# Kernel optimization log

Hardware: AMD Instinct MI355X
Metric: run time of the kernel (lower is better)

Reference implementation:

```python
import jax, jax.numpy as jnp
import numpy as np

N = 50000      # nodes
E = 800000     # edges
C = 128        # dim_feat / channels
D = 256        # dim_dense
OUT = 2        # dim_out
L = 5          # num_layers - 1 GCN2Conv layers
ALPHA = 0.1    # main_param -> GCN2Conv alpha; theta=None -> beta=1.0
SLOPE = 0.01   # LeakyReLU default negative slope


def setup_inputs() -> dict:
    key = jax.random.key(0)
    ks = jax.random.split(key, 6)
    x = jax.random.normal(ks[0], (N, C), jnp.float32)
    edge_index = jax.random.randint(ks[1], (2, E), 0, N, jnp.int32)
    conv_weights = jax.random.normal(ks[2], (L, C, C), jnp.float32) * (1.0 / np.sqrt(C))
    w_dense = jax.random.normal(ks[3], (C, D), jnp.float32) * (1.0 / np.sqrt(C))
    b_dense = jnp.zeros((D,), jnp.float32)
    w_out = jax.random.normal(ks[4], (D, OUT), jnp.float32) * (1.0 / np.sqrt(D))
    b_out = jnp.zeros((OUT,), jnp.float32)
    return dict(x=x, edge_index=edge_index, conv_weights=conv_weights,
                w_dense=w_dense, b_dense=b_dense, w_out=w_out, b_out=b_out)


def _gcn_norm(edge_index, num_nodes):
    """Symmetric gcn_norm with self-loops: returns row, col, D^-1/2 * D^-1/2 edge weights."""
    loop = jnp.arange(num_nodes, dtype=edge_index.dtype)
    row = jnp.concatenate([edge_index[0], loop])  # sources
    col = jnp.concatenate([edge_index[1], loop])  # targets (aggregation index)
    ones = jnp.ones(row.shape[0], jnp.float32)
    deg = jax.ops.segment_sum(ones, col, num_segments=num_nodes)
    dinv = jnp.where(deg > 0, jax.lax.rsqrt(jnp.maximum(deg, 1e-12)), 0.0)
    return row, col, dinv[row] * dinv[col]


def reference(x, edge_index, conv_weights, w_dense, b_dense, w_out, b_out):
    num_nodes = x.shape[0]
    row, col, norm = _gcn_norm(edge_index, num_nodes)
    x0 = x
    for l in range(conv_weights.shape[0]):
        # propagate: h[i] = sum_{j->i} norm * x[j]   (gather -> scatter-add)
        h = jax.ops.segment_sum(norm[:, None] * x[row], col, num_segments=num_nodes)
        # GCN2Conv with shared_weights=True, beta=1 (theta=None): out = ((1-a)h + a*x0) @ W
        out = (1.0 - ALPHA) * h + ALPHA * x0
        x = jax.nn.leaky_relu(out @ conv_weights[l], negative_slope=SLOPE)
    x = x @ w_dense + b_dense
    return x @ w_out + b_out
```

## Files before the change

kernel.cpp:

```cpp
#include <hip/hip_runtime.h>
#include <hip/hip_fp16.h>

#define C 128
#define NOUT 2
#define ALPHA 0.1f
#define SLOPE 0.01f
#define ZP 136

typedef _Float16 half4v __attribute__((ext_vector_type(4)));
typedef float float4v __attribute__((ext_vector_type(4)));


__global__ void count_kernel(const int* __restrict__ col, int* __restrict__ cnt,
                             int* __restrict__ rank, int E) {
    int e = blockIdx.x * 256 + threadIdx.x;
    if (e < E) rank[e] = atomicAdd(&cnt[col[e]], 1);
}

__global__ __launch_bounds__(1024) void scanA_kernel(const int* __restrict__ cnt,
                                                     int* __restrict__ offs,
                                                     int* __restrict__ bsum,
                                                     float* __restrict__ dinv, int n) {
    __shared__ int wsum[16];
    int t = threadIdx.x, lane = t & 63, wv = t >> 6;
    int i = blockIdx.x * 1024 + t;
    int v = (i < n) ? cnt[i] : 0;
    if (i < n) dinv[i] = rsqrtf((float)(v + 1));
    int sc = v;
    #pragma unroll
    for (int d = 1; d < 64; d <<= 1) {
        int u = __shfl_up(sc, d);
        if (lane >= d) sc += u;
    }
    if (lane == 63) wsum[wv] = sc;
    __syncthreads();
    int woff = 0;
    #pragma unroll
    for (int j = 0; j < 16; ++j) woff += (j < wv) ? wsum[j] : 0;
    if (i < n) offs[i] = woff + sc - v;
    if (t == 0) {
        int tot = 0;
        #pragma unroll
        for (int j = 0; j < 16; ++j) tot += wsum[j];
        bsum[blockIdx.x] = tot;
    }
}

__global__ __launch_bounds__(1024) void scanB_kernel(const int* __restrict__ bsum,
                                                     int* __restrict__ bbase, int nb) {
    __shared__ int wsum[16];
    int t = threadIdx.x, lane = t & 63, wv = t >> 6;
    int v = (t < nb) ? bsum[t] : 0;
    int sc = v;
    #pragma unroll
    for (int d = 1; d < 64; d <<= 1) {
        int u = __shfl_up(sc, d);
        if (lane >= d) sc += u;
    }
    if (lane == 63) wsum[wv] = sc;
    __syncthreads();
    int woff = 0;
    #pragma unroll
    for (int j = 0; j < 16; ++j) woff += (j < wv) ? wsum[j] : 0;
    if (t < nb) bbase[t] = woff + sc - v;
}

__global__ void scanC_kernel(int* __restrict__ offs, const int* __restrict__ bbase,
                             int n, int E) {
    int i = blockIdx.x * 256 + threadIdx.x;
    if (i < n) offs[i] = offs[i] + bbase[i >> 10];
    if (i == n) offs[n] = E;
}

__global__ void fill_kernel(const int* __restrict__ row, const int* __restrict__ col,
                            const float* __restrict__ dinv, const int* __restrict__ offs,
                            const int* __restrict__ rank, unsigned* __restrict__ csr, int E) {
    int base = blockIdx.x * 2048 + threadIdx.x;
    #pragma unroll
    for (int j = 0; j < 8; ++j) {
        int e = base + j * 256;
        if (e < E) {
            int r = row[e], c = col[e];
            union { __half h; unsigned short u; } nh;
            nh.h = __float2half_rn(dinv[r] * dinv[c]);
            csr[offs[c] + rank[e]] = ((unsigned)r << 16) | (unsigned)nh.u;
        }
    }
}

__global__ __launch_bounds__(256) void convert_kernel(const float* __restrict__ x,
                                                      __half* __restrict__ xh, int n) {
    int g = blockIdx.x * 256 + threadIdx.x;
    if (g >= n * 32) return;
    float4 v = ((const float4*)x)[g];
    union { __half2 h; unsigned u; } a, b;
    a.h = __float22half2_rn(make_float2(v.x, v.y));
    b.h = __float22half2_rn(make_float2(v.z, v.w));
    ((uint2*)xh)[g] = make_uint2(a.u, b.u);
}

__global__ void wtc_kernel(const float* __restrict__ W, _Float16* __restrict__ WT, int total) {
    int idx = blockIdx.x * 256 + threadIdx.x;
    if (idx >= total) return;
    int l = idx >> 14, rem = idx & 16383;
    int nrow = rem >> 7, kk = rem & 127;
    WT[idx] = (_Float16)W[(l << 14) + kk * C + nrow];
}

__global__ void wdc_kernel(const float* __restrict__ wd, _Float16* __restrict__ WDT) {
    int idx = blockIdx.x * 256 + threadIdx.x;
    if (idx >= 256 * C) return;
    int nrow = idx >> 7, kk = idx & 127;
    WDT[idx] = (_Float16)wd[kk * 256 + nrow];
}

__device__ __forceinline__ void accum8(float* a, uint4 q, float w) {
    union { unsigned u; __half2 h; } c;
    float2 f;
    c.u = q.x; f = __half22float2(c.h); a[0] += w * f.x; a[1] += w * f.y;
    c.u = q.y; f = __half22float2(c.h); a[2] += w * f.x; a[3] += w * f.y;
    c.u = q.z; f = __half22float2(c.h); a[4] += w * f.x; a[5] += w * f.y;
    c.u = q.w; f = __half22float2(c.h); a[6] += w * f.x; a[7] += w * f.y;
}

__device__ __forceinline__ uint4 pack8(const float* a) {
    union { __half2 h; unsigned u; } c0, c1, c2, c3;
    c0.h = __float22half2_rn(make_float2(a[0], a[1]));
    c1.h = __float22half2_rn(make_float2(a[2], a[3]));
    c2.h = __float22half2_rn(make_float2(a[4], a[5]));
    c3.h = __float22half2_rn(make_float2(a[6], a[7]));
    return make_uint4(c0.u, c1.u, c2.u, c3.u);
}

__device__ __forceinline__ float norm_of(unsigned m) {
    union { unsigned short u; __half h; } nh;
    nh.u = (unsigned short)(m & 0xffffu);
    return __half2float(nh.h);
}

__global__ __launch_bounds__(256) void agg_kernel(
    const __half* __restrict__ xc, const __half* __restrict__ x0h,
    const int* __restrict__ offs, const unsigned* __restrict__ csr,
    const float* __restrict__ dinv, __half* __restrict__ z, int n)
{
    int node = blockIdx.x * 8 + (threadIdx.x >> 5);
    if (node >= n) return;
    int l32 = threadIdx.x & 31;
    int sub = l32 >> 4;
    int cg = l32 & 15;
    const uint4* x4 = (const uint4*)xc;
    float a0[8] = {}, a1[8] = {}, a2[8] = {}, a3[8] = {};
    int beg = offs[node], end = offs[node + 1];
    int k = beg + sub;
    for (; k + 14 < end; k += 16) {
        unsigned m0 = csr[k], m1 = csr[k + 2], m2 = csr[k + 4], m3 = csr[k + 6];
        unsigned m4 = csr[k + 8], m5 = csr[k + 10], m6 = csr[k + 12], m7 = csr[k + 14];
        uint4 q0 = x4[(size_t)(m0 >> 16) * 16 + cg];
        uint4 q1 = x4[(size_t)(m1 >> 16) * 16 + cg];
        uint4 q2 = x4[(size_t)(m2 >> 16) * 16 + cg];
        uint4 q3 = x4[(size_t)(m3 >> 16) * 16 + cg];
        uint4 q4 = x4[(size_t)(m4 >> 16) * 16 + cg];
        uint4 q5 = x4[(size_t)(m5 >> 16) * 16 + cg];
        uint4 q6 = x4[(size_t)(m6 >> 16) * 16 + cg];
        uint4 q7 = x4[(size_t)(m7 >> 16) * 16 + cg];
        accum8(a0, q0, norm_of(m0));
        accum8(a1, q1, norm_of(m1));
        accum8(a2, q2, norm_of(m2));
        accum8(a3, q3, norm_of(m3));
        accum8(a0, q4, norm_of(m4));
        accum8(a1, q5, norm_of(m5));
        accum8(a2, q6, norm_of(m6));
        accum8(a3, q7, norm_of(m7));
    }
    for (; k + 6 < end; k += 8) {
        unsigned m0 = csr[k], m1 = csr[k + 2], m2 = csr[k + 4], m3 = csr[k + 6];
        uint4 q0 = x4[(size_t)(m0 >> 16) * 16 + cg];
        uint4 q1 = x4[(size_t)(m1 >> 16) * 16 + cg];
        uint4 q2 = x4[(size_t)(m2 >> 16) * 16 + cg];
        uint4 q3 = x4[(size_t)(m3 >> 16) * 16 + cg];
        accum8(a0, q0, norm_of(m0));
        accum8(a1, q1, norm_of(m1));
        accum8(a2, q2, norm_of(m2));
        accum8(a3, q3, norm_of(m3));
    }
    for (; k < end; k += 2) {
        unsigned m = csr[k];
        uint4 q = x4[(size_t)(m >> 16) * 16 + cg];
        accum8(a0, q, norm_of(m));
    }
    #pragma unroll
    for (int j = 0; j < 8; ++j) a0[j] += a1[j] + a2[j] + a3[j];
    #pragma unroll
    for (int j = 0; j < 8; ++j) a0[j] += __shfl_xor(a0[j], 16);
    if (sub == 0) {
        float di = dinv[node], sw = di * di;
        uint4 qs = x4[(size_t)node * 16 + cg];
        accum8(a0, qs, sw);
        uint4 q0x = ((const uint4*)x0h)[(size_t)node * 16 + cg];
        float xr[8] = {};
        accum8(xr, q0x, 1.f);
        float zz[8];
        #pragma unroll
        for (int j = 0; j < 8; ++j) zz[j] = (1.f - ALPHA) * a0[j] + ALPHA * xr[j];
        ((uint4*)z)[(size_t)node * 16 + cg] = pack8(zz);
    }
}

__global__ __launch_bounds__(256) void layer_mfma(
    const __half* __restrict__ zin, const _Float16* __restrict__ WT,
    __half* __restrict__ xn, int n)
{
    __shared__ _Float16 zl[64 * ZP];
    __shared__ _Float16 ol[64 * ZP];
    int i0 = blockIdx.x * 64;
    int t = threadIdx.x;
    int w = t >> 6, lane = t & 63;
    int c = lane & 15, g = lane >> 4;

    const uint4* z4 = (const uint4*)zin;
    for (int p = t; p < 64 * 16; p += 256) {
        int r = p >> 4, c8 = p & 15;
        uint4 zv = make_uint4(0, 0, 0, 0);
        if (i0 + r < n) zv = z4[(size_t)(i0 + r) * 16 + c8];
        *(uint4*)&zl[r * ZP + c8 * 8] = zv;
    }

    half4v bf[8][2];
    #pragma unroll
    for (int kb = 0; kb < 8; ++kb)
        #pragma unroll
        for (int nt = 0; nt < 2; ++nt)
            bf[kb][nt] = *(const half4v*)&WT[((w * 2 + nt) * 16 + c) * C + kb * 16 + 4 * g];

    __syncthreads();

    #pragma unroll
    for (int m = 0; m < 4; ++m) {
        const _Float16* arow = &zl[(m * 16 + c) * ZP];
        half4v af[8];
        #pragma unroll
        for (int kb = 0; kb < 8; ++kb) af[kb] = *(const half4v*)&arow[kb * 16 + 4 * g];
        float4v acc0 = (float4v)0.f, acc1 = (float4v)0.f;
        #pragma unroll
        for (int kb = 0; kb < 8; ++kb) {
            acc0 = __builtin_amdgcn_mfma_f32_16x16x16f16(af[kb], bf[kb][0], acc0, 0, 0, 0);
            acc1 = __builtin_amdgcn_mfma_f32_16x16x16f16(af[kb], bf[kb][1], acc1, 0, 0, 0);
        }
        #pragma unroll
        for (int r = 0; r < 4; ++r) {
            float v0 = acc0[r]; v0 = v0 > 0.f ? v0 : SLOPE * v0;
            float v1 = acc1[r]; v1 = v1 > 0.f ? v1 : SLOPE * v1;
            ol[(m * 16 + 4 * g + r) * ZP + (w * 2 + 0) * 16 + c] = (_Float16)v0;
            ol[(m * 16 + 4 * g + r) * ZP + (w * 2 + 1) * 16 + c] = (_Float16)v1;
        }
    }
    __syncthreads();
    for (int p = t; p < 64 * 16; p += 256) {
        int r = p >> 4, c8 = p & 15;
        int node = i0 + r;
        if (node < n)
            ((uint4*)xn)[(size_t)node * 16 + c8] = *(uint4*)&ol[r * ZP + c8 * 8];
    }
}

__global__ __launch_bounds__(256) void dense_mfma(
    const __half* __restrict__ xin, const _Float16* __restrict__ WDT,
    const float* __restrict__ bd, const float* __restrict__ wo,
    const float* __restrict__ bo, float* __restrict__ out, int n)
{
    __shared__ _Float16 xl[64 * ZP];
    __shared__ float pp[64][4][2];
    int i0 = blockIdx.x * 64;
    int t = threadIdx.x;
    int w = t >> 6, lane = t & 63;
    int c = lane & 15, g = lane >> 4;

    const uint4* g4 = (const uint4*)xin;
    for (int p = t; p < 64 * 16; p += 256) {
        int r = p >> 4, c8 = p & 15;
        uint4 v = make_uint4(0, 0, 0, 0);
        if (i0 + r < n) v = g4[(size_t)(i0 + r) * 16 + c8];
        *(uint4*)&xl[r * ZP + c8 * 8] = v;
    }

    half4v bf[8][4];
    #pragma unroll
    for (int kb = 0; kb < 8; ++kb)
        #pragma unroll
        for (int nt = 0; nt < 4; ++nt)
            bf[kb][nt] = *(const half4v*)&WDT[((w * 4 + nt) * 16 + c) * C + kb * 16 + 4 * g];
    float bdv[4], wo0[4], wo1[4];
    #pragma unroll
    for (int nt = 0; nt < 4; ++nt) {
        int coln = (w * 4 + nt) * 16 + c;
        bdv[nt] = bd[coln];
        wo0[nt] = wo[coln * 2 + 0];
        wo1[nt] = wo[coln * 2 + 1];
    }

    __syncthreads();

    #pragma unroll
    for (int m = 0; m < 4; ++m) {
        const _Float16* arow = &xl[(m * 16 + c) * ZP];
        half4v af[8];
        #pragma unroll
        for (int kb = 0; kb < 8; ++kb) af[kb] = *(const half4v*)&arow[kb * 16 + 4 * g];
        float4v acc[4];
        #pragma unroll
        for (int nt = 0; nt < 4; ++nt) acc[nt] = (float4v)0.f;
        #pragma unroll
        for (int kb = 0; kb < 8; ++kb) {
            #pragma unroll
            for (int nt = 0; nt < 4; ++nt)
                acc[nt] = __builtin_amdgcn_mfma_f32_16x16x16f16(af[kb], bf[kb][nt], acc[nt], 0, 0, 0);
        }
        float p0[4] = {0.f, 0.f, 0.f, 0.f}, p1[4] = {0.f, 0.f, 0.f, 0.f};
        #pragma unroll
        for (int nt = 0; nt < 4; ++nt) {
            #pragma unroll
            for (int r = 0; r < 4; ++r) {
                float hv = acc[nt][r] + bdv[nt];
                p0[r] += hv * wo0[nt];
                p1[r] += hv * wo1[nt];
            }
        }
        #pragma unroll
        for (int ms = 1; ms <= 8; ms <<= 1) {
            #pragma unroll
            for (int r = 0; r < 4; ++r) {
                p0[r] += __shfl_xor(p0[r], ms);
                p1[r] += __shfl_xor(p1[r], ms);
            }
        }
        if (c == 0) {
            #pragma unroll
            for (int r = 0; r < 4; ++r) {
                pp[m * 16 + 4 * g + r][w][0] = p0[r];
                pp[m * 16 + 4 * g + r][w][1] = p1[r];
            }
        }
    }
    __syncthreads();
    if (t < 128) {
        int r = t >> 1, o = t & 1;
        int node = i0 + r;
        if (node < n) {
            float s = pp[r][0][o] + pp[r][1][o] + pp[r][2][o] + pp[r][3][o];
            out[(size_t)node * NOUT + o] = s + bo[o];
        }
    }
}

extern "C" void kernel_launch(void* const* d_in, const int* in_sizes, int n_in,
                              void* d_out, int out_size, void* d_ws, size_t ws_size,
                              hipStream_t stream) {
    const float* x0    = (const float*)d_in[0];
    const int*   ei    = (const int*)d_in[1];
    const float* convW = (const float*)d_in[2];
    const float* wd    = (const float*)d_in[3];
    const float* bd    = (const float*)d_in[4];
    const float* wo    = (const float*)d_in[5];
    const float* bo    = (const float*)d_in[6];
    float* out = (float*)d_out;

    int N = in_sizes[0] / C;
    int E = in_sizes[1] / 2;
    int L = in_sizes[2] / (C * C);
    const int* row = ei;
    const int* col = ei + E;
    int NB = (N + 1023) / 1024;

    char* p = (char*)d_ws;
    auto alloc = [&](size_t bytes) {
        char* r = p;
        p += (bytes + 255) & ~(size_t)255;
        return r;
    };
    int*      cnt    = (int*)alloc((size_t)N * 4);
    int*      offs   = (int*)alloc((size_t)(N + 1) * 4);
    int*      rank   = (int*)alloc((size_t)E * 4);
    int*      bsum   = (int*)alloc((size_t)NB * 4);
    int*      bbase  = (int*)alloc((size_t)NB * 4);
    unsigned* csr    = (unsigned*)alloc((size_t)E * 4);
    float*    dinv   = (float*)alloc((size_t)N * 4);
    __half*   x0h    = (__half*)alloc((size_t)N * C * 2);
    __half*   bufA   = (__half*)alloc((size_t)N * C * 2);
    __half*   zbuf   = (__half*)alloc((size_t)N * C * 2);
    _Float16* WT     = (_Float16*)alloc((size_t)L * C * C * 2);
    _Float16* WDT    = (_Float16*)alloc((size_t)256 * C * 2);

    hipMemsetAsync(cnt, 0, (size_t)N * 4, stream);
    count_kernel<<<(E + 255) / 256, 256, 0, stream>>>(col, cnt, rank, E);
    scanA_kernel<<<NB, 1024, 0, stream>>>(cnt, offs, bsum, dinv, N);
    scanB_kernel<<<1, 1024, 0, stream>>>(bsum, bbase, NB);
    scanC_kernel<<<(N + 256) / 256, 256, 0, stream>>>(offs, bbase, N, E);
    fill_kernel<<<(E + 2047) / 2048, 256, 0, stream>>>(row, col, dinv, offs, rank, csr, E);
    convert_kernel<<<(N * 32 + 255) / 256, 256, 0, stream>>>(x0, x0h, N);
    int wtot = L * C * C;
    wtc_kernel<<<(wtot + 255) / 256, 256, 0, stream>>>(convW, WT, wtot);
    wdc_kernel<<<(256 * C + 255) / 256, 256, 0, stream>>>(wd, WDT);

    const __half* xc = x0h;
    for (int l = 0; l < L; ++l) {
        agg_kernel<<<(N + 7) / 8, 256, 0, stream>>>(xc, x0h, offs, csr, dinv, zbuf, N);
        layer_mfma<<<(N + 63) / 64, 256, 0, stream>>>(zbuf, WT + (size_t)l * C * C,
                                                      bufA, N);
        xc = bufA;
    }
    dense_mfma<<<(N + 63) / 64, 256, 0, stream>>>(xc, WDT, bd, wo, bo, out, N);
}
```

Measured before the change: 365.8 us.

## Merge prep kernels, hoist agg self loads, widen layer_mfma to 512 threads

Folds the scan-finalize, fp32-to-fp16 conversion and both weight-transpose kernels into one prep launch that picks its role by block index, removing three launches. In the aggregation kernel the self-row, x0 row and dinv loads are issued before the edge loop so their latency overlaps the gathers. layer_mfma moves to 512 threads with 8 waves, each computing one 16-column tile instead of two, which trades per-wave MFMA work and register use for more waves per block.

```diff
diff --git a/kernel.cpp b/kernel.cpp
--- a/kernel.cpp
+++ b/kernel.cpp
@@ -65,11 +65,38 @@
     if (t < nb) bbase[t] = woff + sc - v;
 }
 
-__global__ void scanC_kernel(int* __restrict__ offs, const int* __restrict__ bbase,
-                             int n, int E) {
-    int i = blockIdx.x * 256 + threadIdx.x;
-    if (i < n) offs[i] = offs[i] + bbase[i >> 10];
-    if (i == n) offs[n] = E;
+__global__ __launch_bounds__(256) void prep_kernel(
+    int* __restrict__ offs, const int* __restrict__ bbase, int n, int E,
+    const float* __restrict__ x, __half* __restrict__ xh,
+    const float* __restrict__ W, _Float16* __restrict__ WT, int wtot,
+    const float* __restrict__ wd, _Float16* __restrict__ WDT,
+    int SC, int CV, int WTB)
+{
+    int b = blockIdx.x;
+    if (b < SC) {
+        int i = b * 256 + threadIdx.x;
+        if (i < n) offs[i] = offs[i] + bbase[i >> 10];
+        if (i == n) offs[n] = E;
+    } else if (b < SC + CV) {
+        int g = (b - SC) * 256 + threadIdx.x;
+        if (g >= n * 32) return;
+        float4 v = ((const float4*)x)[g];
+        union { __half2 h; unsigned u; } a2, b2;
+        a2.h = __float22half2_rn(make_float2(v.x, v.y));
+        b2.h = __float22half2_rn(make_float2(v.z, v.w));
+        ((uint2*)xh)[g] = make_uint2(a2.u, b2.u);
+    } else if (b < SC + CV + WTB) {
+        int idx = (b - SC - CV) * 256 + threadIdx.x;
+        if (idx >= wtot) return;
+        int l = idx >> 14, rem = idx & 16383;
+        int nrow = rem >> 7, kk = rem & 127;
+        WT[idx] = (_Float16)W[(l << 14) + kk * C + nrow];
+    } else {
+        int idx = (b - SC - CV - WTB) * 256 + threadIdx.x;
+        if (idx >= 256 * C) return;
+        int nrow = idx >> 7, kk = idx & 127;
+        WDT[idx] = (_Float16)wd[kk * 256 + nrow];
+    }
 }
 
 __global__ void fill_kernel(const int* __restrict__ row, const int* __restrict__ col,
@@ -86,32 +113,6 @@
             csr[offs[c] + rank[e]] = ((unsigned)r << 16) | (unsigned)nh.u;
         }
     }
-}
-
-__global__ __launch_bounds__(256) void convert_kernel(const float* __restrict__ x,
-                                                      __half* __restrict__ xh, int n) {
-    int g = blockIdx.x * 256 + threadIdx.x;
-    if (g >= n * 32) return;
-    float4 v = ((const float4*)x)[g];
-    union { __half2 h; unsigned u; } a, b;
-    a.h = __float22half2_rn(make_float2(v.x, v.y));
-    b.h = __float22half2_rn(make_float2(v.z, v.w));
-    ((uint2*)xh)[g] = make_uint2(a.u, b.u);
-}
-
-__global__ void wtc_kernel(const float* __restrict__ W, _Float16* __restrict__ WT, int total) {
-    int idx = blockIdx.x * 256 + threadIdx.x;
-    if (idx >= total) return;
-    int l = idx >> 14, rem = idx & 16383;
-    int nrow = rem >> 7, kk = rem & 127;
-    WT[idx] = (_Float16)W[(l << 14) + kk * C + nrow];
-}
-
-__global__ void wdc_kernel(const float* __restrict__ wd, _Float16* __restrict__ WDT) {
-    int idx = blockIdx.x * 256 + threadIdx.x;
-    if (idx >= 256 * C) return;
-    int nrow = idx >> 7, kk = idx & 127;
-    WDT[idx] = (_Float16)wd[kk * 256 + nrow];
 }
 
 __device__ __forceinline__ void accum8(float* a, uint4 q, float w) {
@@ -149,6 +150,10 @@
     int sub = l32 >> 4;
     int cg = l32 & 15;
     const uint4* x4 = (const uint4*)xc;
+    uint4 qs = x4[(size_t)node * 16 + cg];
+    uint4 q0x = ((const uint4*)x0h)[(size_t)node * 16 + cg];
+    float di = dinv[node];
+
     float a0[8] = {}, a1[8] = {}, a2[8] = {}, a3[8] = {};
     int beg = offs[node], end = offs[node + 1];
     int k = beg + sub;
@@ -193,10 +198,8 @@
     #pragma unroll
     for (int j = 0; j < 8; ++j) a0[j] += __shfl_xor(a0[j], 16);
     if (sub == 0) {
-        float di = dinv[node], sw = di * di;
-        uint4 qs = x4[(size_t)node * 16 + cg];
+        float sw = di * di;
         accum8(a0, qs, sw);
-        uint4 q0x = ((const uint4*)x0h)[(size_t)node * 16 + cg];
         float xr[8] = {};
         accum8(xr, q0x, 1.f);
         float zz[8];
@@ -206,7 +209,7 @@
     }
 }
 
-__global__ __launch_bounds__(256) void layer_mfma(
+__global__ __launch_bounds__(512) void layer_mfma(
     const __half* __restrict__ zin, const _Float16* __restrict__ WT,
     __half* __restrict__ xn, int n)
 {
@@ -218,19 +221,18 @@
     int c = lane & 15, g = lane >> 4;
 
     const uint4* z4 = (const uint4*)zin;
-    for (int p = t; p < 64 * 16; p += 256) {
+    #pragma unroll
+    for (int p = t; p < 64 * 16; p += 512) {
         int r = p >> 4, c8 = p & 15;
         uint4 zv = make_uint4(0, 0, 0, 0);
         if (i0 + r < n) zv = z4[(size_t)(i0 + r) * 16 + c8];
         *(uint4*)&zl[r * ZP + c8 * 8] = zv;
     }
 
-    half4v bf[8][2];
+    half4v bf[8];
     #pragma unroll
     for (int kb = 0; kb < 8; ++kb)
-        #pragma unroll
-        for (int nt = 0; nt < 2; ++nt)
-            bf[kb][nt] = *(const half4v*)&WT[((w * 2 + nt) * 16 + c) * C + kb * 16 + 4 * g];
+        bf[kb] = *(const half4v*)&WT[(w * 16 + c) * C + kb * 16 + 4 * g];
 
     __syncthreads();
 
@@ -240,22 +242,20 @@
         half4v af[8];
         #pragma unroll
         for (int kb = 0; kb < 8; ++kb) af[kb] = *(const half4v*)&arow[kb * 16 + 4 * g];
-        float4v acc0 = (float4v)0.f, acc1 = (float4v)0.f;
-        #pragma unroll
-        for (int kb = 0; kb < 8; ++kb) {
-            acc0 = __builtin_amdgcn_mfma_f32_16x16x16f16(af[kb], bf[kb][0], acc0, 0, 0, 0);
-            acc1 = __builtin_amdgcn_mfma_f32_16x16x16f16(af[kb], bf[kb][1], acc1, 0, 0, 0);
-        }
+        float4v acc = (float4v)0.f;
+        #pragma unroll
+        for (int kb = 0; kb < 8; ++kb)
+            acc = __builtin_amdgcn_mfma_f32_16x16x16f16(af[kb], bf[kb], acc, 0, 0, 0);
         #pragma unroll
         for (int r = 0; r < 4; ++r) {
-            float v0 = acc0[r]; v0 = v0 > 0.f ? v0 : SLOPE * v0;
-            float v1 = acc1[r]; v1 = v1 > 0.f ? v1 : SLOPE * v1;
-            ol[(m * 16 + 4 * g + r) * ZP + (w * 2 + 0) * 16 + c] = (_Float16)v0;
-            ol[(m * 16 + 4 * g + r) * ZP + (w * 2 + 1) * 16 + c] = (_Float16)v1;
-        }
-    }
-    __syncthreads();
-    for (int p = t; p < 64 * 16; p += 256) {
+            float v = acc[r];
+            v = v > 0.f ? v : SLOPE * v;
+            ol[(m * 16 + 4 * g + r) * ZP + w * 16 + c] = (_Float16)v;
+        }
+    }
+    __syncthreads();
+    #pragma unroll
+    for (int p = t; p < 64 * 16; p += 512) {
         int r = p >> 4, c8 = p & 15;
         int node = i0 + r;
         if (node < n)
@@ -394,17 +394,19 @@
     count_kernel<<<(E + 255) / 256, 256, 0, stream>>>(col, cnt, rank, E);
     scanA_kernel<<<NB, 1024, 0, stream>>>(cnt, offs, bsum, dinv, N);
     scanB_kernel<<<1, 1024, 0, stream>>>(bsum, bbase, NB);
-    scanC_kernel<<<(N + 256) / 256, 256, 0, stream>>>(offs, bbase, N, E);
+    int wtot = L * C * C;
+    int SC  = (N + 256) / 256;
+    int CV  = (N * 32 + 255) / 256;
+    int WTB = (wtot + 255) / 256;
+    int WDB = (256 * C + 255) / 256;
+    prep_kernel<<<SC + CV + WTB + WDB, 256, 0, stream>>>(
+        offs, bbase, N, E, x0, x0h, convW, WT, wtot, wd, WDT, SC, CV, WTB);
     fill_kernel<<<(E + 2047) / 2048, 256, 0, stream>>>(row, col, dinv, offs, rank, csr, E);
-    convert_kernel<<<(N * 32 + 255) / 256, 256, 0, stream>>>(x0, x0h, N);
-    int wtot = L * C * C;
-    wtc_kernel<<<(wtot + 255) / 256, 256, 0, stream>>>(convW, WT, wtot);
-    wdc_kernel<<<(256 * C + 255) / 256, 256, 0, stream>>>(wd, WDT);
 
     const __half* xc = x0h;
     for (int l = 0; l < L; ++l) {
         agg_kernel<<<(N + 7) / 8, 256, 0, stream>>>(xc, x0h, offs, csr, dinv, zbuf, N);
-        layer_mfma<<<(N + 63) / 64, 256, 0, stream>>>(zbuf, WT + (size_t)l * C * C,
+        layer_mfma<<<(N + 63) / 64, 512, 0, stream>>>(zbuf, WT + (size_t)l * C * C,
                                                       bufA, N);
         xc = bufA;
     }
```

Result: no change. 366.0 us (+0.1%).

## Merge setup kernels into one launch, hoist self loads, store layer output directly

Applied to the files above, without the earlier changes.

Folds the edge counting, x-to-half conversion and the two weight transposes into a single multi-role kernel, dispatched by block index, to cut three launches from the prologue. The aggregation kernel now issues its self-row, x0-row and dinv loads before the edge loop so their latency overlaps the gathers. The layer GEMM kernel drops its output shared-memory staging and second barrier and writes half values straight to global memory. Those direct writes are scattered 2-byte stores rather than coalesced 16-byte rows, which can raise write traffic inefficiency.

```diff
diff --git a/kernel.cpp b/kernel.cpp
--- a/kernel.cpp
+++ b/kernel.cpp
@@ -11,10 +11,41 @@
 typedef float float4v __attribute__((ext_vector_type(4)));
 
 
-__global__ void count_kernel(const int* __restrict__ col, int* __restrict__ cnt,
-                             int* __restrict__ rank, int E) {
-    int e = blockIdx.x * 256 + threadIdx.x;
-    if (e < E) rank[e] = atomicAdd(&cnt[col[e]], 1);
+__global__ __launch_bounds__(256) void count_prep_kernel(
+    const int* __restrict__ col, int* __restrict__ cnt, int* __restrict__ rank, int E,
+    const float* __restrict__ x, __half* __restrict__ xh, int n,
+    const float* __restrict__ W, _Float16* __restrict__ WT, int wtot,
+    const float* __restrict__ wd, _Float16* __restrict__ WDT,
+    int CB, int CV, int WTB)
+{
+    int b = blockIdx.x;
+    if (b < CB) {
+        int base = b * 1024 + threadIdx.x;
+        #pragma unroll
+        for (int j = 0; j < 4; ++j) {
+            int e = base + j * 256;
+            if (e < E) rank[e] = atomicAdd(&cnt[col[e]], 1);
+        }
+    } else if (b < CB + CV) {
+        int g = (b - CB) * 256 + threadIdx.x;
+        if (g >= n * 32) return;
+        float4 v = ((const float4*)x)[g];
+        union { __half2 h; unsigned u; } a2, b2;
+        a2.h = __float22half2_rn(make_float2(v.x, v.y));
+        b2.h = __float22half2_rn(make_float2(v.z, v.w));
+        ((uint2*)xh)[g] = make_uint2(a2.u, b2.u);
+    } else if (b < CB + CV + WTB) {
+        int idx = (b - CB - CV) * 256 + threadIdx.x;
+        if (idx >= wtot) return;
+        int l = idx >> 14, rem = idx & 16383;
+        int nrow = rem >> 7, kk = rem & 127;
+        WT[idx] = (_Float16)W[(l << 14) + kk * C + nrow];
+    } else {
+        int idx = (b - CB - CV - WTB) * 256 + threadIdx.x;
+        if (idx >= 256 * C) return;
+        int nrow = idx >> 7, kk = idx & 127;
+        WDT[idx] = (_Float16)wd[kk * 256 + nrow];
+    }
 }
 
 __global__ __launch_bounds__(1024) void scanA_kernel(const int* __restrict__ cnt,
@@ -86,32 +117,6 @@
             csr[offs[c] + rank[e]] = ((unsigned)r << 16) | (unsigned)nh.u;
         }
     }
-}
-
-__global__ __launch_bounds__(256) void convert_kernel(const float* __restrict__ x,
-                                                      __half* __restrict__ xh, int n) {
-    int g = blockIdx.x * 256 + threadIdx.x;
-    if (g >= n * 32) return;
-    float4 v = ((const float4*)x)[g];
-    union { __half2 h; unsigned u; } a, b;
-    a.h = __float22half2_rn(make_float2(v.x, v.y));
-    b.h = __float22half2_rn(make_float2(v.z, v.w));
-    ((uint2*)xh)[g] = make_uint2(a.u, b.u);
-}
-
-__global__ void wtc_kernel(const float* __restrict__ W, _Float16* __restrict__ WT, int total) {
-    int idx = blockIdx.x * 256 + threadIdx.x;
-    if (idx >= total) return;
-    int l = idx >> 14, rem = idx & 16383;
-    int nrow = rem >> 7, kk = rem & 127;
-    WT[idx] = (_Float16)W[(l << 14) + kk * C + nrow];
-}
-
-__global__ void wdc_kernel(const float* __restrict__ wd, _Float16* __restrict__ WDT) {
-    int idx = blockIdx.x * 256 + threadIdx.x;
-    if (idx >= 256 * C) return;
-    int nrow = idx >> 7, kk = idx & 127;
-    WDT[idx] = (_Float16)wd[kk * 256 + nrow];
 }
 
 __device__ __forceinline__ void accum8(float* a, uint4 q, float w) {
@@ -149,6 +154,10 @@
     int sub = l32 >> 4;
     int cg = l32 & 15;
     const uint4* x4 = (const uint4*)xc;
+    uint4 qs = x4[(size_t)node * 16 + cg];
+    uint4 q0x = ((const uint4*)x0h)[(size_t)node * 16 + cg];
+    float di = dinv[node];
+
     float a0[8] = {}, a1[8] = {}, a2[8] = {}, a3[8] = {};
     int beg = offs[node], end = offs[node + 1];
     int k = beg + sub;
@@ -193,10 +202,8 @@
     #pragma unroll
     for (int j = 0; j < 8; ++j) a0[j] += __shfl_xor(a0[j], 16);
     if (sub == 0) {
-        float di = dinv[node], sw = di * di;
-        uint4 qs = x4[(size_t)node * 16 + cg];
+        float sw = di * di;
         accum8(a0, qs, sw);
-        uint4 q0x = ((const uint4*)x0h)[(size_t)node * 16 + cg];
         float xr[8] = {};
         accum8(xr, q0x, 1.f);
         float zz[8];
@@ -211,13 +218,13 @@
     __half* __restrict__ xn, int n)
 {
     __shared__ _Float16 zl[64 * ZP];
-    __shared__ _Float16 ol[64 * ZP];
     int i0 = blockIdx.x * 64;
     int t = threadIdx.x;
     int w = t >> 6, lane = t & 63;
     int c = lane & 15, g = lane >> 4;
 
     const uint4* z4 = (const uint4*)zin;
+    #pragma unroll
     for (int p = t; p < 64 * 16; p += 256) {
         int r = p >> 4, c8 = p & 15;
         uint4 zv = make_uint4(0, 0, 0, 0);
@@ -248,18 +255,14 @@
         }
         #pragma unroll
         for (int r = 0; r < 4; ++r) {
-            float v0 = acc0[r]; v0 = v0 > 0.f ? v0 : SLOPE * v0;
-            float v1 = acc1[r]; v1 = v1 > 0.f ? v1 : SLOPE * v1;
-            ol[(m * 16 + 4 * g + r) * ZP + (w * 2 + 0) * 16 + c] = (_Float16)v0;
-            ol[(m * 16 + 4 * g + r) * ZP + (w * 2 + 1) * 16 + c] = (_Float16)v1;
-        }
-    }
-    __syncthreads();
-    for (int p = t; p < 64 * 16; p += 256) {
-        int r = p >> 4, c8 = p & 15;
-        int node = i0 + r;
-        if (node < n)
-            ((uint4*)xn)[(size_t)node * 16 + c8] = *(uint4*)&ol[r * ZP + c8 * 8];
+            int node = i0 + m * 16 + 4 * g + r;
+            if (node < n) {
+                float v0 = acc0[r]; v0 = v0 > 0.f ? v0 : SLOPE * v0;
+                float v1 = acc1[r]; v1 = v1 > 0.f ? v1 : SLOPE * v1;
+                xn[(size_t)node * C + w * 32 + c]      = __float2half_rn(v0);
+                xn[(size_t)node * C + w * 32 + 16 + c] = __float2half_rn(v1);
+            }
+        }
     }
 }
 
@@ -390,16 +393,19 @@
     _Float16* WT     = (_Float16*)alloc((size_t)L * C * C * 2);
     _Float16* WDT    = (_Float16*)alloc((size_t)256 * C * 2);
 
+    int wtot = L * C * C;
+    int CB  = (E + 1023) / 1024;
+    int CV  = (N * 32 + 255) / 256;
+    int WTB = (wtot + 255) / 256;
+    int WDB = (256 * C + 255) / 256;
+
     hipMemsetAsync(cnt, 0, (size_t)N * 4, stream);
-    count_kernel<<<(E + 255) / 256, 256, 0, stream>>>(col, cnt, rank, E);
+    count_prep_kernel<<<CB + CV + WTB + WDB, 256, 0, stream>>>(
+        col, cnt, rank, E, x0, x0h, N, convW, WT, wtot, wd, WDT, CB, CV, WTB);
     scanA_kernel<<<NB, 1024, 0, stream>>>(cnt, offs, bsum, dinv, N);
     scanB_kernel<<<1, 1024, 0, stream>>>(bsum, bbase, NB);
     scanC_kernel<<<(N + 256) / 256, 256, 0, stream>>>(offs, bbase, N, E);
     fill_kernel<<<(E + 2047) / 2048, 256, 0, stream>>>(row, col, dinv, offs, rank, csr, E);
-    convert_kernel<<<(N * 32 + 255) / 256, 256, 0, stream>>>(x0, x0h, N);
-    int wtot = L * C * C;
-    wtc_kernel<<<(wtot + 255) / 256, 256, 0, stream>>>(convW, WT, wtot);
-    wdc_kernel<<<(256 * C + 255) / 256, 256, 0, stream>>>(wd, WDT);
 
     const __half* xc = x0h;
     for (int l = 0; l < L; ++l) {
```

After: 368.5 us. About the same (+0.7%).
